# Kernel tuning notes

Measured on AMD Instinct MI355X. Metric: run time of the kernel, lower is better.

Reference implementation:

```python
import jax, jax.numpy as jnp
import numpy as np

HEADS = 16
LN_EPS = 1e-5


def setup_inputs() -> dict:
    key = jax.random.key(0)
    ks = jax.random.split(key, 4)
    B, S, C, U = 2, 2048, 1024, 1024
    scale = 1.0 / np.sqrt(C)
    return {
        "inputs": jax.random.normal(ks[0], (B, S, C), dtype=jnp.float32),
        "Wq": jax.random.normal(ks[1], (C, U), dtype=jnp.float32) * scale,
        "bq": jnp.zeros((U,), dtype=jnp.float32),
        "Wk": jax.random.normal(ks[2], (C, U), dtype=jnp.float32) * scale,
        "bk": jnp.zeros((U,), dtype=jnp.float32),
        "Wv": jax.random.normal(ks[3], (C, U), dtype=jnp.float32) * scale,
        "bv": jnp.zeros((U,), dtype=jnp.float32),
        "ln_gamma": jnp.ones((S, U), dtype=jnp.float32),
        "ln_beta": jnp.zeros((S, U), dtype=jnp.float32),
    }


def reference(inputs, Wq, bq, Wk, bk, Wv, bv, ln_gamma, ln_beta):
    B, S, C = inputs.shape
    U = Wq.shape[1]
    H = HEADS
    dh = U // H

    Q = inputs @ Wq + bq  # [B,S,U]
    K = inputs @ Wk + bk
    V = inputs @ Wv + bv

    # torch: concat(split(X, U//H, dim=-1), dim=0) -> head-major stacking on batch
    def split_heads(X):
        return jnp.moveaxis(X.reshape(B, S, H, dh), 2, 0).reshape(H * B, S, dh)

    Q_, K_, V_ = split_heads(Q), split_heads(K), split_heads(V)

    scores = jnp.einsum('bqd,bkd->bqk', Q_, K_) / jnp.sqrt(jnp.float32(dh))
    tri = jnp.tril(jnp.ones((S, S), dtype=bool))  # causal mask
    scores = jnp.where(tri[None, :, :], scores, jnp.float32(-1e9))
    attn = jax.nn.softmax(scores, axis=-1)
    out_ = jnp.einsum('bqk,bkd->bqd', attn, V_)  # [H*B,S,dh]

    # inverse: split on batch into H chunks of size B, concat on feature dim
    out = jnp.moveaxis(out_.reshape(H, B, S, dh), 0, 2).reshape(B, S, U)

    out = out + inputs  # residual

    # LayerNorm over normalized_shape=[S, U] (joint seq+feature stats)
    mu = jnp.mean(out, axis=(-2, -1), keepdims=True)
    var = jnp.mean(jnp.square(out - mu), axis=(-2, -1), keepdims=True)
    out = (out - mu) / jnp.sqrt(var + LN_EPS) * ln_gamma + ln_beta
    return out
```

## Files before the change

kernel.cpp:

```cpp
#include <hip/hip_runtime.h>
#include <hip/hip_bf16.h>


typedef __bf16 bf16_t;
typedef __bf16 bf16x8 __attribute__((ext_vector_type(8)));
typedef __bf16 bf16x4 __attribute__((ext_vector_type(4)));
typedef _Float16 f16_t;
typedef _Float16 f16x4 __attribute__((ext_vector_type(4)));
typedef _Float16 f16x8 __attribute__((ext_vector_type(8)));
typedef float f32x4 __attribute__((ext_vector_type(4)));

constexpr int Bsz = 2;
constexpr int Seq = 2048;
constexpr int Cdim = 1024;
constexpr int Udim = 1024;
constexpr int Hn = 16;
constexpr int Dh = 64;
constexpr int Mrows = Bsz * Seq;
constexpr int PerBatch = Seq * Udim;

__device__ __forceinline__ void gload16(const void* g, void* l)
{
    __builtin_amdgcn_global_load_lds(
        (const __attribute__((address_space(1))) void*)g,
        (__attribute__((address_space(3))) void*)l, 16, 0, 0);
}

__global__ __launch_bounds__(256)
void cast_x(const float* __restrict__ X, bf16_t* __restrict__ Xb)
{
    int i = blockIdx.x * 256 + threadIdx.x;
    float4 v = ((const float4*)X)[i];
    bf16x4 o = { (bf16_t)v.x, (bf16_t)v.y, (bf16_t)v.z, (bf16_t)v.w };
    *(bf16x4*)(Xb + (size_t)i * 4) = o;
}

__global__ void transpose_w(const float* __restrict__ Wq, const float* __restrict__ Wk,
                            const float* __restrict__ Wv,
                            bf16_t* __restrict__ Tq, bf16_t* __restrict__ Tk,
                            bf16_t* __restrict__ Tv)
{
    int z = blockIdx.z;
    const float* W = (z == 0) ? Wq : (z == 1) ? Wk : Wv;
    bf16_t* T = (z == 0) ? Tq : (z == 1) ? Tk : Tv;
    __shared__ bf16_t t[64][65];
    int x0 = blockIdx.x * 64, y0 = blockIdx.y * 64;
    int tx = threadIdx.x;
    for (int i = threadIdx.y; i < 64; i += 8)
        t[i][tx] = (bf16_t)W[(size_t)(y0 + i) * Cdim + x0 + tx];
    __syncthreads();
    for (int i = threadIdx.y; i < 64; i += 8)
        T[(size_t)(x0 + i) * Cdim + y0 + tx] = t[tx][i];
}

__global__ __launch_bounds__(256)
void gemm_qkv(const bf16_t* __restrict__ X,
              const bf16_t* __restrict__ Wt0, const bf16_t* __restrict__ Wt1,
              const bf16_t* __restrict__ Wt2,
              const float* __restrict__ b0, const float* __restrict__ b1,
              const float* __restrict__ b2,
              f16_t* __restrict__ O0, f16_t* __restrict__ O1, f16_t* __restrict__ O2)
{
    int z = blockIdx.z;
    const bf16_t* Wt = (z == 0) ? Wt0 : (z == 1) ? Wt1 : Wt2;
    const float* bias = (z == 0) ? b0 : (z == 1) ? b1 : b2;
    f16_t* Og = (z == 0) ? O0 : (z == 1) ? O1 : O2;

    constexpr int Kd = 1024, Nd = 1024;
    __shared__ __align__(16) bf16_t As[128 * 32];
    __shared__ __align__(16) bf16_t Bs[128 * 32];

    int tid = threadIdx.x;
    int wave = tid >> 6, lane = tid & 63, quad = lane >> 4, l16 = lane & 15;
    int wm = (wave & 1) * 64, wn = (wave >> 1) * 64;
    int m0 = blockIdx.y * 128, n0 = blockIdx.x * 128;

    f32x4 acc[4][4] = {};

    int e0 = wave * 512 + lane * 8;
    int r0 = e0 >> 5, c0 = e0 & 31;
    int e1 = e0 + 2048;
    int r1 = e1 >> 5, c1 = e1 & 31;
    const bf16_t* Ag = X + (size_t)m0 * Kd;
    const bf16_t* Bg = Wt + (size_t)n0 * Kd;
    bf16_t* AsW0 = As + wave * 512;
    bf16_t* AsW1 = As + 2048 + wave * 512;
    bf16_t* BsW0 = Bs + wave * 512;
    bf16_t* BsW1 = Bs + 2048 + wave * 512;

    for (int k0 = 0; k0 < Kd; k0 += 32) {
        gload16(Ag + (size_t)r0 * Kd + k0 + c0, AsW0);
        gload16(Ag + (size_t)r1 * Kd + k0 + c1, AsW1);
        gload16(Bg + (size_t)r0 * Kd + k0 + c0, BsW0);
        gload16(Bg + (size_t)r1 * Kd + k0 + c1, BsW1);
        __syncthreads();

        bf16x8 af[4], bfr[4];
#pragma unroll
        for (int i = 0; i < 4; i++)
            af[i] = *(const bf16x8*)&As[(wm + i * 16 + l16) * 32 + quad * 8];
#pragma unroll
        for (int i = 0; i < 4; i++)
            bfr[i] = *(const bf16x8*)&Bs[(wn + i * 16 + l16) * 32 + quad * 8];
#pragma unroll
        for (int mt = 0; mt < 4; mt++)
#pragma unroll
            for (int nt = 0; nt < 4; nt++)
                acc[mt][nt] = __builtin_amdgcn_mfma_f32_16x16x32_bf16(
                    af[mt], bfr[nt], acc[mt][nt], 0, 0, 0);
        __syncthreads();
    }

#pragma unroll
    for (int nt = 0; nt < 4; nt++) {
        int col = n0 + wn + nt * 16 + l16;
        float bv = bias[col];
#pragma unroll
        for (int mt = 0; mt < 4; mt++) {
            int row = m0 + wm + mt * 16 + quad * 4;
#pragma unroll
            for (int r = 0; r < 4; r++)
                Og[(size_t)(row + r) * Nd + col] = (f16_t)(acc[mt][nt][r] + bv);
        }
    }
}

__global__ void transpose_v(const f16_t* __restrict__ V, f16_t* __restrict__ Vt)
{
    int s0 = blockIdx.x * 64;
    int y = blockIdx.y;
    int b = y >> 4, h = y & 15;
    __shared__ f16_t t[64][65];
    int tx = threadIdx.x;
    for (int i = threadIdx.y; i < 64; i += 8)
        t[i][tx] = V[(size_t)(b * Seq + s0 + i) * Udim + h * Dh + tx];
    __syncthreads();
    for (int i = threadIdx.y; i < 64; i += 8)
        Vt[((size_t)y * Dh + i) * Seq + s0 + tx] = t[tx][i];
}

__global__ __launch_bounds__(256)
void attn4(const f16_t* __restrict__ Q, const f16_t* __restrict__ K,
           const f16_t* __restrict__ Vt, const float* __restrict__ X,
           float* __restrict__ R, float* __restrict__ stats)
{
    int p = blockIdx.x, h = blockIdx.y, b = blockIdx.z;
    int tid = threadIdx.x;
    int w = tid >> 6, lane = tid & 63, quad = lane >> 4, l16 = lane & 15;
    size_t bS = (size_t)b * Seq;

    __shared__ f16_t Ks[64][72];
    __shared__ f16_t Vs[64][72];

    const f16_t* Kg = K + bS * Udim + h * Dh;
    const f16_t* Vg = Vt + ((size_t)(b * Hn + h)) * Dh * Seq;

    float s_acc = 0.0f, ss_acc = 0.0f;
    int sr = tid >> 2, sc = (tid & 3) * 16;

#pragma unroll
    for (int pass = 0; pass < 2; pass++) {
        int qtile = pass ? (31 - p) : p;
        int q0 = qtile * 64 + w * 16;
        int qidx = q0 + l16;

        const f16_t* Qp = Q + (bS + qidx) * Udim + h * Dh;
        f16x8 qf[2];
#pragma unroll
        for (int s = 0; s < 2; s++) qf[s] = *(const f16x8*)(Qp + s * 32 + quad * 8);

        f32x4 Oacc[4] = {};
        float m = -1e30f, l = 0.0f;

        for (int kv0 = 0; kv0 <= qtile * 64; kv0 += 64) {
            {
                const f16_t* kp = Kg + (size_t)(kv0 + sr) * Udim + sc;
                f16x8 k0 = *(const f16x8*)kp;
                f16x8 k1 = *(const f16x8*)(kp + 8);
                const f16_t* vp = Vg + (size_t)sr * Seq + kv0 + sc;
                f16x8 v0 = *(const f16x8*)vp;
                f16x8 v1 = *(const f16x8*)(vp + 8);
                *(f16x8*)&Ks[sr][sc] = k0;
                *(f16x8*)&Ks[sr][sc + 8] = k1;
                *(f16x8*)&Vs[sr][sc] = v0;
                *(f16x8*)&Vs[sr][sc + 8] = v1;
            }
            __syncthreads();

            bool diag = (kv0 == qtile * 64);

            f32x4 st[4];
#pragma unroll
            for (int t = 0; t < 4; t++) {
                f32x4 a = {};
#pragma unroll
                for (int s = 0; s < 2; s++) {
                    f16x8 kf = *(const f16x8*)&Ks[t * 16 + l16][s * 32 + quad * 8];
                    a = __builtin_amdgcn_mfma_f32_16x16x32_f16(kf, qf[s], a, 0, 0, 0);
                }
                st[t] = a;
            }

            float mx = -1e30f;
#pragma unroll
            for (int t = 0; t < 4; t++)
#pragma unroll
                for (int r = 0; r < 4; r++) {
                    float sv = st[t][r] * 0.125f;
                    if (diag && (kv0 + t * 16 + quad * 4 + r > qidx))
                        sv = -1e30f;
                    st[t][r] = sv;
                    mx = fmaxf(mx, sv);
                }
            mx = fmaxf(mx, __shfl_xor(mx, 16));
            mx = fmaxf(mx, __shfl_xor(mx, 32));
            float mnew = fmaxf(m, mx);
            float alpha = __expf(m - mnew);
            float sum = 0.0f;
            f16x4 pf[4];
#pragma unroll
            for (int t = 0; t < 4; t++)
#pragma unroll
                for (int r = 0; r < 4; r++) {
                    float pv = __expf(st[t][r] - mnew);
                    sum += pv;
                    pf[t][r] = (f16_t)pv;
                }
            sum += __shfl_xor(sum, 16);
            sum += __shfl_xor(sum, 32);
            l = l * alpha + sum;
            m = mnew;
#pragma unroll
            for (int dt = 0; dt < 4; dt++)
#pragma unroll
                for (int r = 0; r < 4; r++) Oacc[dt][r] *= alpha;

#pragma unroll
            for (int dt = 0; dt < 4; dt++) {
#pragma unroll
                for (int t = 0; t < 4; t++) {
                    f16x4 vf = *(const f16x4*)&Vs[dt * 16 + l16][t * 16 + quad * 4];
                    Oacc[dt] = __builtin_amdgcn_mfma_f32_16x16x16f16(vf, pf[t], Oacc[dt], 0, 0, 0);
                }
            }
            __syncthreads();
        }

        float invl = 1.0f / l;
        const float* Xp = X + (bS + qidx) * Udim + h * Dh;
        float* Rp = R + (bS + qidx) * Udim + h * Dh;
#pragma unroll
        for (int dt = 0; dt < 4; dt++) {
            f32x4 xv = *(const f32x4*)(Xp + dt * 16 + quad * 4);
            f32x4 o = Oacc[dt] * invl + xv;
            *(f32x4*)(Rp + dt * 16 + quad * 4) = o;
#pragma unroll
            for (int r = 0; r < 4; r++) {
                s_acc += o[r];
                ss_acc += o[r] * o[r];
            }
        }
    }

#pragma unroll
    for (int o = 1; o < 64; o <<= 1) {
        s_acc += __shfl_xor(s_acc, o);
        ss_acc += __shfl_xor(ss_acc, o);
    }
    __shared__ float red[8];
    if (lane == 0) { red[w] = s_acc; red[4 + w] = ss_acc; }
    __syncthreads();
    if (tid == 0) {
        atomicAdd(&stats[b], red[0] + red[1] + red[2] + red[3]);
        atomicAdd(&stats[2 + b], red[4] + red[5] + red[6] + red[7]);
    }
}

__global__ __launch_bounds__(256)
void ln_norm(const float* __restrict__ R, const float* __restrict__ gamma,
             const float* __restrict__ beta, const float* __restrict__ stats,
             float* __restrict__ out)
{
    constexpr int TOT4 = Bsz * Seq * Udim / 4;
    constexpr float invN = 1.0f / (float)PerBatch;
    float mu[2], inv[2];
    for (int b = 0; b < 2; b++) {
        float m = stats[b] * invN;
        float var = stats[2 + b] * invN - m * m;
        mu[b] = m;
        inv[b] = rsqrtf(var + 1e-5f);
    }
    for (int i = blockIdx.x * blockDim.x + threadIdx.x; i < TOT4;
         i += gridDim.x * blockDim.x) {
        int f = i * 4;
        int b = f >> 21;
        int su = f & (PerBatch - 1);
        float4 rv = *(const float4*)(R + f);
        float4 g = *(const float4*)(gamma + su);
        float4 be = *(const float4*)(beta + su);
        float4 o;
        o.x = (rv.x - mu[b]) * inv[b] * g.x + be.x;
        o.y = (rv.y - mu[b]) * inv[b] * g.y + be.y;
        o.z = (rv.z - mu[b]) * inv[b] * g.z + be.z;
        o.w = (rv.w - mu[b]) * inv[b] * g.w + be.w;
        *(float4*)(out + f) = o;
    }
}

extern "C" void kernel_launch(void* const* d_in, const int* in_sizes, int n_in,
                              void* d_out, int out_size, void* d_ws, size_t ws_size,
                              hipStream_t stream)
{
    const float* X     = (const float*)d_in[0];
    const float* Wq    = (const float*)d_in[1];
    const float* bq    = (const float*)d_in[2];
    const float* Wk    = (const float*)d_in[3];
    const float* bk    = (const float*)d_in[4];
    const float* Wv    = (const float*)d_in[5];
    const float* bv    = (const float*)d_in[6];
    const float* gamma = (const float*)d_in[7];
    const float* beta  = (const float*)d_in[8];
    float* out = (float*)d_out;

    char* ws = (char*)d_ws;
    size_t off = 0;
    auto alloc = [&](size_t bytes) -> void* {
        void* p = ws + off;
        off += (bytes + 255) & ~(size_t)255;
        return p;
    };
    bf16_t* Xb = (bf16_t*)alloc((size_t)Mrows * Cdim * 2);
    bf16_t* Tq = (bf16_t*)alloc((size_t)Cdim * Udim * 2);
    bf16_t* Tk = (bf16_t*)alloc((size_t)Cdim * Udim * 2);
    bf16_t* Tv = (bf16_t*)alloc((size_t)Cdim * Udim * 2);
    f16_t*  Qb = (f16_t*)alloc((size_t)Mrows * Udim * 2);
    f16_t*  Kb = (f16_t*)alloc((size_t)Mrows * Udim * 2);
    f16_t*  Vb = (f16_t*)alloc((size_t)Mrows * Udim * 2);
    f16_t*  Vtb = (f16_t*)alloc((size_t)Mrows * Udim * 2);
    float*  Rb = (float*)alloc((size_t)Mrows * Udim * 4);
    float*  stats = (float*)alloc(4 * sizeof(float));

    hipMemsetAsync(stats, 0, 4 * sizeof(float), stream);
    cast_x<<<dim3(Mrows * Cdim / 4 / 256), 256, 0, stream>>>(X, Xb);
    transpose_w<<<dim3(16, 16, 3), dim3(64, 8), 0, stream>>>(Wq, Wk, Wv, Tq, Tk, Tv);
    gemm_qkv<<<dim3(8, 32, 3), 256, 0, stream>>>(Xb, Tq, Tk, Tv, bq, bk, bv, Qb, Kb, Vb);
    transpose_v<<<dim3(Seq / 64, Bsz * Hn), dim3(64, 8), 0, stream>>>(Vb, Vtb);
    attn4<<<dim3(16, Hn, Bsz), 256, 0, stream>>>(Qb, Kb, Vtb, X, Rb, stats);
    ln_norm<<<dim3(1024), 256, 0, stream>>>(Rb, gamma, beta, stats, out);
}
```

Before: 216.4 us.

## Double-buffer K/V tiles in attention, skip masked diagonal MFMAs, remap blocks

The attention kernel now prefetches the next K/V tile into registers while computing on the current one, and writes it into a second shared-memory buffer. This overlaps global loads with MFMA work and removes one barrier per iteration. On the diagonal tile, 16-key subtiles that lie entirely above the causal boundary for a wave are no longer computed. The softmax folds log2(e) into the scale and uses exp2f. The grid becomes 1-D with a remapped block order that groups heads, likely to improve K/V cache locality. The cost is doubled LDS use, more live registers, and some branch divergence on the diagonal.

```diff
diff --git a/kernel.cpp b/kernel.cpp
--- a/kernel.cpp
+++ b/kernel.cpp
@@ -140,27 +140,34 @@
 }
 
 __global__ __launch_bounds__(256)
-void attn4(const f16_t* __restrict__ Q, const f16_t* __restrict__ K,
+void attn5(const f16_t* __restrict__ Q, const f16_t* __restrict__ K,
            const f16_t* __restrict__ Vt, const float* __restrict__ X,
            float* __restrict__ R, float* __restrict__ stats)
 {
-    int p = blockIdx.x, h = blockIdx.y, b = blockIdx.z;
+    int id = blockIdx.x;
+    int c = id & 7, g = id >> 3;
+    int p = g & 15, mhi = g >> 4;
+    int bh = (mhi << 3) | c;
+    int b = bh >> 4, h = bh & 15;
+
     int tid = threadIdx.x;
     int w = tid >> 6, lane = tid & 63, quad = lane >> 4, l16 = lane & 15;
     size_t bS = (size_t)b * Seq;
 
-    __shared__ f16_t Ks[64][72];
-    __shared__ f16_t Vs[64][72];
+    __shared__ f16_t Ks[2][64][72];
+    __shared__ f16_t Vs[2][64][72];
 
     const f16_t* Kg = K + bS * Udim + h * Dh;
     const f16_t* Vg = Vt + ((size_t)(b * Hn + h)) * Dh * Seq;
 
     float s_acc = 0.0f, ss_acc = 0.0f;
     int sr = tid >> 2, sc = (tid & 3) * 16;
+    constexpr float SCL = 0.125f * 1.44269504088896340736f;
 
 #pragma unroll
     for (int pass = 0; pass < 2; pass++) {
         int qtile = pass ? (31 - p) : p;
+        int nkv = qtile * 64;
         int q0 = qtile * 64 + w * 16;
         int qidx = q0 + l16;
 
@@ -172,33 +179,49 @@
         f32x4 Oacc[4] = {};
         float m = -1e30f, l = 0.0f;
 
-        for (int kv0 = 0; kv0 <= qtile * 64; kv0 += 64) {
-            {
-                const f16_t* kp = Kg + (size_t)(kv0 + sr) * Udim + sc;
-                f16x8 k0 = *(const f16x8*)kp;
-                f16x8 k1 = *(const f16x8*)(kp + 8);
-                const f16_t* vp = Vg + (size_t)sr * Seq + kv0 + sc;
-                f16x8 v0 = *(const f16x8*)vp;
-                f16x8 v1 = *(const f16x8*)(vp + 8);
-                *(f16x8*)&Ks[sr][sc] = k0;
-                *(f16x8*)&Ks[sr][sc + 8] = k1;
-                *(f16x8*)&Vs[sr][sc] = v0;
-                *(f16x8*)&Vs[sr][sc + 8] = v1;
-            }
-            __syncthreads();
-
-            bool diag = (kv0 == qtile * 64);
+        {
+            const f16_t* kp = Kg + (size_t)sr * Udim + sc;
+            const f16_t* vp = Vg + (size_t)sr * Seq + sc;
+            f16x8 k0 = *(const f16x8*)kp;
+            f16x8 k1 = *(const f16x8*)(kp + 8);
+            f16x8 v0 = *(const f16x8*)vp;
+            f16x8 v1 = *(const f16x8*)(vp + 8);
+            *(f16x8*)&Ks[0][sr][sc] = k0;
+            *(f16x8*)&Ks[0][sr][sc + 8] = k1;
+            *(f16x8*)&Vs[0][sr][sc] = v0;
+            *(f16x8*)&Vs[0][sr][sc + 8] = v1;
+        }
+        __syncthreads();
+
+        int buf = 0;
+        for (int kv0 = 0; kv0 <= nkv; kv0 += 64) {
+            bool have = (kv0 + 64 <= nkv);
+            f16x8 nk0, nk1, nv0, nv1;
+            if (have) {
+                const f16_t* kp = Kg + (size_t)(kv0 + 64 + sr) * Udim + sc;
+                const f16_t* vp = Vg + (size_t)sr * Seq + kv0 + 64 + sc;
+                nk0 = *(const f16x8*)kp;
+                nk1 = *(const f16x8*)(kp + 8);
+                nv0 = *(const f16x8*)vp;
+                nv1 = *(const f16x8*)(vp + 8);
+            }
+
+            bool diag = (kv0 == nkv);
 
             f32x4 st[4];
 #pragma unroll
             for (int t = 0; t < 4; t++) {
-                f32x4 a = {};
-#pragma unroll
-                for (int s = 0; s < 2; s++) {
-                    f16x8 kf = *(const f16x8*)&Ks[t * 16 + l16][s * 32 + quad * 8];
-                    a = __builtin_amdgcn_mfma_f32_16x16x32_f16(kf, qf[s], a, 0, 0, 0);
+                if (!diag || t <= w) {
+                    f32x4 a = {};
+#pragma unroll
+                    for (int s = 0; s < 2; s++) {
+                        f16x8 kf = *(const f16x8*)&Ks[buf][t * 16 + l16][s * 32 + quad * 8];
+                        a = __builtin_amdgcn_mfma_f32_16x16x32_f16(kf, qf[s], a, 0, 0, 0);
+                    }
+                    st[t] = a;
+                } else {
+                    st[t] = f32x4{-1e30f, -1e30f, -1e30f, -1e30f};
                 }
-                st[t] = a;
             }
 
             float mx = -1e30f;
@@ -206,7 +229,7 @@
             for (int t = 0; t < 4; t++)
 #pragma unroll
                 for (int r = 0; r < 4; r++) {
-                    float sv = st[t][r] * 0.125f;
+                    float sv = st[t][r] * SCL;
                     if (diag && (kv0 + t * 16 + quad * 4 + r > qidx))
                         sv = -1e30f;
                     st[t][r] = sv;
@@ -215,14 +238,14 @@
             mx = fmaxf(mx, __shfl_xor(mx, 16));
             mx = fmaxf(mx, __shfl_xor(mx, 32));
             float mnew = fmaxf(m, mx);
-            float alpha = __expf(m - mnew);
+            float alpha = exp2f(m - mnew);
             float sum = 0.0f;
             f16x4 pf[4];
 #pragma unroll
             for (int t = 0; t < 4; t++)
 #pragma unroll
                 for (int r = 0; r < 4; r++) {
-                    float pv = __expf(st[t][r] - mnew);
+                    float pv = exp2f(st[t][r] - mnew);
                     sum += pv;
                     pf[t][r] = (f16_t)pv;
                 }
@@ -236,14 +259,24 @@
                 for (int r = 0; r < 4; r++) Oacc[dt][r] *= alpha;
 
 #pragma unroll
-            for (int dt = 0; dt < 4; dt++) {
-#pragma unroll
-                for (int t = 0; t < 4; t++) {
-                    f16x4 vf = *(const f16x4*)&Vs[dt * 16 + l16][t * 16 + quad * 4];
-                    Oacc[dt] = __builtin_amdgcn_mfma_f32_16x16x16f16(vf, pf[t], Oacc[dt], 0, 0, 0);
+            for (int t = 0; t < 4; t++) {
+                if (!diag || t <= w) {
+#pragma unroll
+                    for (int dt = 0; dt < 4; dt++) {
+                        f16x4 vf = *(const f16x4*)&Vs[buf][dt * 16 + l16][t * 16 + quad * 4];
+                        Oacc[dt] = __builtin_amdgcn_mfma_f32_16x16x16f16(vf, pf[t], Oacc[dt], 0, 0, 0);
+                    }
                 }
             }
+
+            if (have) {
+                *(f16x8*)&Ks[buf ^ 1][sr][sc] = nk0;
+                *(f16x8*)&Ks[buf ^ 1][sr][sc + 8] = nk1;
+                *(f16x8*)&Vs[buf ^ 1][sr][sc] = nv0;
+                *(f16x8*)&Vs[buf ^ 1][sr][sc + 8] = nv1;
+            }
             __syncthreads();
+            buf ^= 1;
         }
 
         float invl = 1.0f / l;
@@ -345,6 +378,6 @@
     transpose_w<<<dim3(16, 16, 3), dim3(64, 8), 0, stream>>>(Wq, Wk, Wv, Tq, Tk, Tv);
     gemm_qkv<<<dim3(8, 32, 3), 256, 0, stream>>>(Xb, Tq, Tk, Tv, bq, bk, bv, Qb, Kb, Vb);
     transpose_v<<<dim3(Seq / 64, Bsz * Hn), dim3(64, 8), 0, stream>>>(Vb, Vtb);
-    attn4<<<dim3(16, Hn, Bsz), 256, 0, stream>>>(Qb, Kb, Vtb, X, Rb, stats);
+    attn5<<<dim3(512), 256, 0, stream>>>(Qb, Kb, Vtb, X, Rb, stats);
     ln_norm<<<dim3(1024), 256, 0, stream>>>(Rb, gamma, beta, stats, out);
 }
```

Result: no change. 220.2 us (+1.8%).
